# Kernel tuning notes

Hardware: AMD Instinct MI355X
Metric: run time of the kernel (lower is better)

## Reference

```python
import jax, jax.numpy as jnp
import numpy as np

D = 256          # input_dim
H = 4            # num_heads
W = 4            # window_size
NUM_SCALES = 3
FRACTAL = 2
NUM_CLASSES = 7


def _pool(t, ksize):
    # reflect-pad along time by ksize//2 each side, then avg_pool1d(kernel=stride=ksize)
    p = ksize // 2
    t = jnp.pad(t, ((0, 0), (p, p), (0, 0)), mode='reflect')
    B, Tp, F = t.shape
    L = Tp // ksize
    return t[:, :L * ksize].reshape(B, L, ksize, F).mean(axis=2)


def _window_attn(q, k, v):
    # windowed multi-head self-attention with zero-pad to a multiple of W
    B, T, F = q.shape
    pad = (-T) % W
    if pad:
        q = jnp.pad(q, ((0, 0), (0, pad), (0, 0)))
        k = jnp.pad(k, ((0, 0), (0, pad), (0, 0)))
        v = jnp.pad(v, ((0, 0), (0, pad), (0, 0)))
    Tp = T + pad
    nw = Tp // W
    hd = F // H
    scale = 1.0 / np.sqrt(hd).astype(np.float32)
    # [B, nw, W, H, hd] -> [B, nw, H, W, hd]
    qh = q.reshape(B, nw, W, H, hd).transpose(0, 1, 3, 2, 4)
    kh = k.reshape(B, nw, W, H, hd).transpose(0, 1, 3, 2, 4)
    vh = v.reshape(B, nw, W, H, hd).transpose(0, 1, 3, 2, 4)
    attn = jnp.einsum('bnhqd,bnhkd->bnhqk', qh, kh) * scale
    attn = jax.nn.softmax(attn, axis=-1)
    out = jnp.einsum('bnhqk,bnhkd->bnhqd', attn, vh)
    out = out.transpose(0, 1, 3, 2, 4).reshape(B, Tp, F)
    return out[:, :T]


def _upsample_nearest(f, out_len):
    # matches torch F.interpolate(mode='nearest'): src = floor(i * in / out)
    in_len = f.shape[1]
    idx = jnp.minimum((jnp.arange(out_len) * in_len) // out_len, in_len - 1)
    return f[:, idx]


def setup_inputs() -> dict:
    key = jax.random.key(0)
    ks = jax.random.split(key, 14)
    s = 1.0 / np.sqrt(D).astype(np.float32)
    inp = {
        'x': jax.random.normal(ks[0], (32, 4096, D), dtype=jnp.float32),
        'Wq': jax.random.normal(ks[1], (D, D), dtype=jnp.float32) * s,
        'bq': jnp.zeros((D,), jnp.float32),
        'Wk': jax.random.normal(ks[2], (D, D), dtype=jnp.float32) * s,
        'bk': jnp.zeros((D,), jnp.float32),
        'Wv': jax.random.normal(ks[3], (D, D), dtype=jnp.float32) * s,
        'bv': jnp.zeros((D,), jnp.float32),
        'Wp': jax.random.normal(ks[4], (D, D), dtype=jnp.float32) * s,
        'bp': jnp.zeros((D,), jnp.float32),
        'Wc1': jax.random.normal(ks[5], (D, D), dtype=jnp.float32) * s,
        'bc1': jnp.zeros((D,), jnp.float32),
        'Wc2': jax.random.normal(ks[6], (D, NUM_CLASSES), dtype=jnp.float32) * s,
        'bc2': jnp.zeros((NUM_CLASSES,), jnp.float32),
    }
    return inp


def reference(x, Wq, bq, Wk, bk, Wv, bv, Wp, bp, Wc1, bc1, Wc2, bc2):
    B, T, F = x.shape
    q = x @ Wq + bq
    k = x @ Wk + bk
    v = x @ Wv + bv
    # multi-scale temporal operator + per-scale fractal windowed attention
    outs = []
    for s_idx in range(1, NUM_SCALES + 1):
        ksize = FRACTAL ** (s_idx - 1)
        if ksize == 1:
            qs, ks_, vs = q, k, v
        else:
            qs, ks_, vs = _pool(q, ksize), _pool(k, ksize), _pool(v, ksize)
        outs.append(_window_attn(qs, ks_, vs))
    # scale mixer: nearest upsample + exact GELU + sum + proj
    summed = sum(jax.nn.gelu(_upsample_nearest(f, T), approximate=False) for f in outs)
    fused = summed @ Wp + bp
    # classifier (dropout inactive in eval)
    h = fused.mean(axis=1)
    h = jax.nn.relu(h @ Wc1 + bc1)
    logits = h @ Wc2 + bc2
    return logits
```

## Files before the change

### kernel.cpp

```cpp
#include <hip/hip_runtime.h>

#define DD 256
#define TT 4096
#define BB 32

typedef __attribute__((ext_vector_type(8))) short short8;
typedef __attribute__((ext_vector_type(4))) float floatx4;

__device__ __forceinline__ unsigned short f2bf(float f) {
    unsigned u = __builtin_bit_cast(unsigned, f);
    unsigned r = u + 0x7FFFu + ((u >> 16) & 1u);
    return (unsigned short)(r >> 16);
}
__device__ __forceinline__ float bf2f(unsigned short h) {
    return __builtin_bit_cast(float, (unsigned)h << 16);
}
__device__ __forceinline__ float2 unpk(unsigned u) {
    float2 r;
    r.x = __builtin_bit_cast(float, u << 16);
    r.y = __builtin_bit_cast(float, u & 0xFFFF0000u);
    return r;
}

#define GLDS16(g, l)                                                        \
    __builtin_amdgcn_global_load_lds(                                       \
        (const __attribute__((address_space(1))) void*)(g),                 \
        (__attribute__((address_space(3))) void*)(l), 16, 0, 0)

__global__ __launch_bounds__(256)
void prep_kernel(const float* __restrict__ X,
                 const float* __restrict__ Wq, const float* __restrict__ Wk,
                 const float* __restrict__ Wv,
                 unsigned short* __restrict__ Xp, unsigned short* __restrict__ Wt,
                 float* __restrict__ acc)
{
    const int bid = blockIdx.x;
    const int tid = threadIdx.x;
    if (bid < 16384) {
        size_t i = ((size_t)bid * 256 + tid) * 8;
        float4 a = *(const float4*)(X + i);
        float4 b = *(const float4*)(X + i + 4);
        short8 o;
        o[0] = (short)f2bf(a.x); o[1] = (short)f2bf(a.y);
        o[2] = (short)f2bf(a.z); o[3] = (short)f2bf(a.w);
        o[4] = (short)f2bf(b.x); o[5] = (short)f2bf(b.y);
        o[6] = (short)f2bf(b.z); o[7] = (short)f2bf(b.w);
        size_t row = i >> 8;
        int k = (int)(i & 255);
        size_t off = (size_t)(k >> 5) * (131072u * 32u) + row * 32 + (k & 31);
        *(short8*)(Xp + off) = o;
    } else if (bid < 16384 + 768) {
        const int wb = bid - 16384;
        const int z = wb >> 8;
        const int k = wb & 255;
        const int n = tid;
        const float* W = (z == 0) ? Wq : (z == 1) ? Wk : Wv;
        float w = W[k * 256 + n];
        unsigned short hi = f2bf(w);
        unsigned short lo = f2bf(w - bf2f(hi));
        size_t base = (size_t)z * 131072;
        size_t off = (size_t)(k >> 5) * 8192 + (size_t)n * 32 + (k & 31);
        Wt[base +         off] = hi;
        Wt[base + 65536 + off] = lo;
    } else {
        for (int i = tid; i < BB * DD; i += 256) acc[i] = 0.f;
    }
}

__global__ __launch_bounds__(256, 3)
void qkv_mfma_kernel(const unsigned short* __restrict__ Xp,
                     const unsigned short* __restrict__ Wt,
                     const float* __restrict__ bq, const float* __restrict__ bk,
                     const float* __restrict__ bv,
                     unsigned short* __restrict__ Q, unsigned short* __restrict__ Kp,
                     unsigned short* __restrict__ V)
{
    const int d = blockIdx.x;
    const int x = d & 7, t = d >> 3;
    const int m = t / 6, zc = t - 6 * m;
    const int z = zc >> 1;
    const int col0 = (zc & 1) * 128;
    const size_t row0 = (size_t)(x + 8 * m) * 128;

    const unsigned short* Wz = Wt + (size_t)z * 131072;
    const float* bias = (z == 0) ? bq : (z == 1) ? bk : bv;
    unsigned short* Y = (z == 0) ? Q : (z == 1) ? Kp : V;

    __shared__ __align__(16) unsigned char smem[49152];

    const int tid = threadIdx.x;
    const int lane = tid & 63, wave = tid >> 6;
    const int wm = wave & 1, wn = wave >> 1;
    const int l15 = lane & 15, lq = lane >> 4;

    floatx4 acc[4][4];
    #pragma unroll
    for (int i = 0; i < 4; ++i)
        #pragma unroll
        for (int j = 0; j < 4; ++j)
            acc[i][j] = (floatx4){0.f, 0.f, 0.f, 0.f};

    auto stage = [&](int p, int pb) {
        unsigned short* As = (unsigned short*)(smem + pb * 8192);
        unsigned short* Bs = (unsigned short*)(smem + 16384 + pb * 16384);
        const unsigned short* Ap = Xp + (size_t)p * (131072u * 32u);
        const unsigned short* Bp = Wz + (size_t)p * 8192;
        #pragma unroll
        for (int it = 0; it < 2; ++it) {
            int flat = it * 256 + tid;
            int mm = flat >> 2, c = flat & 3;
            int sc = c ^ ((mm >> 1) & 3);
            GLDS16(Ap + (row0 + mm) * 32 + sc * 8, As + flat * 8);
        }
        #pragma unroll
        for (int half = 0; half < 2; ++half)
            #pragma unroll
            for (int it = 0; it < 2; ++it) {
                int flat = it * 256 + tid;
                int n = flat >> 2, c = flat & 3;
                int sc = c ^ ((n >> 1) & 3);
                GLDS16(Bp + half * 65536 + (size_t)(col0 + n) * 32 + sc * 8,
                       Bs + half * 4096 + flat * 8);
            }
    };

    stage(0, 0);
    __syncthreads();

    for (int k = 0; k < 8; ++k) {
        const int pb = k & 1;
        if (k < 7) stage(k + 1, pb ^ 1);

        const unsigned short* As = (const unsigned short*)(smem + pb * 8192);
        const unsigned short* Bs = (const unsigned short*)(smem + 16384 + pb * 16384);

        short8 a[4];
        #pragma unroll
        for (int mt = 0; mt < 4; ++mt) {
            int row = wm * 64 + mt * 16 + l15;
            a[mt] = *(const short8*)(As + row * 32 + (lq ^ ((row >> 1) & 3)) * 8);
        }
        #pragma unroll
        for (int nt = 0; nt < 4; ++nt) {
            int nr = wn * 64 + nt * 16 + l15;
            const unsigned short* bp = Bs + nr * 32 + (lq ^ ((nr >> 1) & 3)) * 8;
            short8 bh = *(const short8*)bp;
            short8 bl = *(const short8*)(bp + 4096);
            #pragma unroll
            for (int mt = 0; mt < 4; ++mt) {
                acc[mt][nt] = __builtin_amdgcn_mfma_f32_16x16x32_bf16(a[mt], bh, acc[mt][nt], 0, 0, 0);
                acc[mt][nt] = __builtin_amdgcn_mfma_f32_16x16x32_bf16(a[mt], bl, acc[mt][nt], 0, 0, 0);
            }
        }
        __syncthreads();
    }

    unsigned short* Cs = (unsigned short*)(smem + wave * 8192);
    #pragma unroll
    for (int nt = 0; nt < 4; ++nt) {
        float bv_ = bias[col0 + wn * 64 + nt * 16 + l15];
        #pragma unroll
        for (int mt = 0; mt < 4; ++mt)
            #pragma unroll
            for (int r = 0; r < 4; ++r) {
                int row = mt * 16 + lq * 4 + r;
                Cs[row * 64 + nt * 16 + l15] = f2bf(acc[mt][nt][r] + bv_);
            }
    }
    #pragma unroll
    for (int p = 0; p < 8; ++p) {
        int row = p * 8 + (lane >> 3);
        float4 dd = *(const float4*)(Cs + row * 64 + (lane & 7) * 8);
        *(float4*)(Y + (row0 + wm * 64 + row) * 256 + col0 + wn * 64 + (lane & 7) * 8) = dd;
    }
}

__device__ __forceinline__ float gelu2(float x) {
    float z = fabsf(x) * 0.70710678118654752f;
    float t = __builtin_amdgcn_rcpf(fmaf(z, 0.3275911f, 1.0f));
    float p = fmaf(t, 1.061405429f, -1.453152027f);
    p = fmaf(p, t, 1.421413741f);
    p = fmaf(p, t, -0.284496736f);
    p = fmaf(p, t, 0.254829592f);
    p = p * t;
    float e = __expf(-z * z);
    float erf_abs = fmaf(-p, e, 1.0f);
    float erfv = copysignf(erf_abs, x);
    return x * (1.0f + erfv);
}
__device__ __forceinline__ void addu4(uint4 d, float* f) {
    float2 t;
    t = unpk(d.x); f[0] += t.x; f[1] += t.y;
    t = unpk(d.y); f[2] += t.x; f[3] += t.y;
    t = unpk(d.z); f[4] += t.x; f[5] += t.y;
    t = unpk(d.w); f[6] += t.x; f[7] += t.y;
}

#define SPAN 32
#define NROW 34

template<int KS>
__device__ __forceinline__ void pool_qk(const unsigned short* __restrict__ qb,
                                        const unsigned short* __restrict__ kb,
                                        int rp,
                                        float* __restrict__ qf,
                                        float* __restrict__ kf)
{
    #pragma unroll
    for (int j = 0; j < KS; ++j) {
        int ra = (rp >> (8 * j)) & 0xFF;
        uint4 qd = *(const uint4*)(qb + ra * 256);
        uint4 kd = *(const uint4*)(kb + ra * 256);
        addu4(qd, qf);
        addu4(kd, kf);
    }
}

template<int KS>
__device__ __forceinline__ void pool_v(const unsigned short* __restrict__ vb,
                                       int rp, float* __restrict__ vf)
{
    #pragma unroll
    for (int j = 0; j < KS; ++j) {
        int ra = (rp >> (8 * j)) & 0xFF;
        uint4 vd = *(const uint4*)(vb + ra * 256);
        addu4(vd, vf);
    }
}

template<int KS>
__device__ __forceinline__ void fast_unit(const unsigned short* __restrict__ qkvs,
                                          int rowbase,
                                          const float* __restrict__ cwh,
                                          float sscale, float inv_k, int fperm,
                                          float* __restrict__ accL)
{
    float S[4][4];
    #pragma unroll
    for (int i = 0; i < 4; ++i)
        #pragma unroll
        for (int j = 0; j < 4; ++j) S[i][j] = 0.f;

    #pragma unroll
    for (int half = 0; half < 2; ++half) {
        const unsigned short* qb = qkvs + half * 128 + fperm + rowbase * 256;
        const unsigned short* kb = qb + NROW * 256;
        float qf[4][8], kf[4][8];
        #pragma unroll
        for (int i = 0; i < 4; ++i) {
            #pragma unroll
            for (int e = 0; e < 8; ++e) { qf[i][e] = 0.f; kf[i][e] = 0.f; }
            #pragma unroll
            for (int j = 0; j < KS; ++j) {
                addu4(*(const uint4*)(qb + (i * KS + j) * 256), qf[i]);
                addu4(*(const uint4*)(kb + (i * KS + j) * 256), kf[i]);
            }
        }
        #pragma unroll
        for (int i = 0; i < 4; ++i)
            #pragma unroll
            for (int j = 0; j < 4; ++j) {
                float d = 0.f;
                #pragma unroll
                for (int e = 0; e < 8; ++e) d = fmaf(qf[i][e], kf[j][e], d);
                S[i][j] += d;
            }
    }
    #pragma unroll
    for (int i = 0; i < 4; ++i)
        #pragma unroll
        for (int j = 0; j < 4; ++j) {
            float t = S[i][j];
            t += __shfl_xor(t, 1, 64);
            t += __shfl_xor(t, 2, 64);
            S[i][j] = t * sscale;
        }
    float P[4][4];
    #pragma unroll
    for (int i = 0; i < 4; ++i) {
        float m = fmaxf(fmaxf(S[i][0], S[i][1]), fmaxf(S[i][2], S[i][3]));
        float e0 = __expf(S[i][0] - m), e1 = __expf(S[i][1] - m);
        float e2 = __expf(S[i][2] - m), e3 = __expf(S[i][3] - m);
        float inv = inv_k * __builtin_amdgcn_rcpf(e0 + e1 + e2 + e3);
        P[i][0] = e0 * inv; P[i][1] = e1 * inv; P[i][2] = e2 * inv; P[i][3] = e3 * inv;
    }
    #pragma unroll
    for (int half = 0; half < 2; ++half) {
        const unsigned short* vb =
            qkvs + 2 * NROW * 256 + half * 128 + fperm + rowbase * 256;
        float vf[4][8];
        #pragma unroll
        for (int i = 0; i < 4; ++i) {
            #pragma unroll
            for (int e = 0; e < 8; ++e) vf[i][e] = 0.f;
            #pragma unroll
            for (int j = 0; j < KS; ++j)
                addu4(*(const uint4*)(vb + (i * KS + j) * 256), vf[i]);
        }
        #pragma unroll
        for (int i = 0; i < 4; ++i) {
            #pragma unroll
            for (int e = 0; e < 8; ++e) {
                float o = P[i][0]*vf[0][e] + P[i][1]*vf[1][e]
                        + P[i][2]*vf[2][e] + P[i][3]*vf[3][e];
                accL[half * 8 + e] += cwh[i] * gelu2(o);
            }
        }
    }
}

__global__ __launch_bounds__(256, 3)
void attn_fused_kernel(const unsigned short* __restrict__ Q,
                       const unsigned short* __restrict__ K,
                       const unsigned short* __restrict__ V,
                       float* __restrict__ acc)
{
    __shared__ __align__(16) unsigned char smem[3 * NROW * 256 * 2];
    unsigned short* qkvs = (unsigned short*)smem;
    float* scratch = (float*)smem;

    const int tid = threadIdx.x;
    const int s = blockIdx.x;
    const int b = blockIdx.y;
    const int r0 = s * SPAN;
    const int rbase = r0 - 2;

    #pragma unroll
    for (int t = 0; t < 3; ++t) {
        const unsigned short* src =
            ((t == 0) ? Q : (t == 1) ? K : V) + (size_t)b * TT * DD;
        #pragma unroll
        for (int it = 0; it < 5; ++it) {
            int flat = it * 256 + tid;
            if (flat < NROW * 32) {
                int row = flat >> 5, dc = flat & 31;
                int g = rbase + row;
                g = (g < 0) ? 0 : g;
                int c = (((dc >> 2) & 3) << 3) | ((dc & 3) << 1) | ((dc >> 4) & 1);
                GLDS16(src + (size_t)g * DD + c * 8,
                       qkvs + t * (NROW * 256) + flat * 8);
            }
        }
    }
    __syncthreads();

    const int slot = tid >> 2, lq = tid & 3;
    const int head = slot & 3, u = slot >> 2;
    int ksize, LEN, w; bool active = true;
    if (u < 8)       { ksize = 1; LEN = 4096; w = s * 8 + u; }
    else if (u < 12) { ksize = 2; LEN = 2049; w = s * 4 + (u - 8); }
    else if (u < 14) { ksize = 4; LEN = 1025; w = s * 2 + (u - 12); }
    else if (u == 14){ ksize = 2; LEN = 2049; w = 512; active = (s == 127); }
    else             { ksize = 4; LEN = 1025; w = 256; active = (s == 127); }

    const int f0 = head * 64 + lq * 16;
    const int fperm = head * 32 + lq * 8;

    float accL[16];
    #pragma unroll
    for (int e = 0; e < 16; ++e) accL[e] = 0.f;

    const bool generic = (s == 0) || (s == 127);

    if (!generic) {
        if (active) {
            float cwh[4];
            if (ksize == 1) {
                #pragma unroll
                for (int i = 0; i < 4; ++i) cwh[i] = 0.5f;
                fast_unit<1>(qkvs, u * 4 + 2, cwh, 0.125f, 1.0f, fperm, accL);
            } else if (ksize == 2) {
                #pragma unroll
                for (int i = 0; i < 4; ++i) {
                    int p = 16 * s + 4 * (u - 8) + i;
                    cwh[i] = 0.5f * (float)(((p + 1) * TT + 2048) / 2049
                                          - (p * TT + 2048) / 2049);
                }
                fast_unit<2>(qkvs, 8 * (u - 8) + 1, cwh, 0.03125f, 0.5f, fperm, accL);
            } else {
                #pragma unroll
                for (int i = 0; i < 4; ++i) {
                    int p = 8 * s + 4 * (u - 12) + i;
                    cwh[i] = 0.5f * (float)(((p + 1) * TT + 1024) / 1025
                                          - (p * TT + 1024) / 1025);
                }
                fast_unit<4>(qkvs, 16 * (u - 12), cwh, 0.0078125f, 0.25f, fperm, accL);
            }
        }
    } else if (active) {
        int rp[4]; float cwh[4]; int vmask = 0;
        for (int i = 0; i < 4; ++i) {
            int p = w * 4 + i;
            bool vv = (p < LEN);
            if (vv) vmask |= (1 << i);
            int pc = vv ? p : 0;
            int r[4] = {0, 0, 0, 0};
            if (ksize == 1) { r[0] = pc; }
            else if (ksize == 2) {
                if (pc == 0)            { r[0] = 0;      r[1] = 1;      }
                else if (pc == LEN - 1) { r[0] = TT - 2; r[1] = TT - 1; }
                else                    { r[0] = 2 * pc - 1; r[1] = 2 * pc; }
            } else {
                if (pc == 0)            { r[0] = 2; r[1] = 1; r[2] = 0; r[3] = 1; }
                else if (pc == LEN - 1) { r[0] = TT - 3; r[1] = TT - 2; r[2] = TT - 2; r[3] = TT - 1; }
                else                    { r[0] = 4*pc - 2; r[1] = 4*pc - 1; r[2] = 4*pc; r[3] = 4*pc + 1; }
            }
            int rr = 0;
            #pragma unroll
            for (int j = 0; j < 4; ++j) rr |= ((r[j] - rbase) & 0xFF) << (8 * j);
            rp[i] = rr;
            float c = 0.5f;
            if (ksize == 2)
                c = 0.5f * (float)(((p + 1) * TT + 2048) / 2049 - (p * TT + 2048) / 2049);
            else if (ksize == 4)
                c = 0.5f * (float)(((p + 1) * TT + 1024) / 1025 - (p * TT + 1024) / 1025);
            cwh[i] = vv ? c : 0.f;
        }
        const float inv_k = 1.0f / (float)ksize;
        const float sscale = 0.125f * inv_k * inv_k;

        float S[4][4];
        #pragma unroll
        for (int i = 0; i < 4; ++i)
            #pragma unroll
            for (int j = 0; j < 4; ++j) S[i][j] = 0.f;

        for (int half = 0; half < 2; ++half) {
            float qf[4][8], kf[4][8];
            const unsigned short* qb = qkvs + half * 128 + fperm;
            const unsigned short* kb = qb + NROW * 256;
            #pragma unroll
            for (int i = 0; i < 4; ++i) {
                #pragma unroll
                for (int e = 0; e < 8; ++e) { qf[i][e] = 0.f; kf[i][e] = 0.f; }
                if (vmask & (1 << i)) {
                    if (ksize == 1)      pool_qk<1>(qb, kb, rp[i], qf[i], kf[i]);
                    else if (ksize == 2) pool_qk<2>(qb, kb, rp[i], qf[i], kf[i]);
                    else                 pool_qk<4>(qb, kb, rp[i], qf[i], kf[i]);
                }
            }
            #pragma unroll
            for (int i = 0; i < 4; ++i)
                #pragma unroll
                for (int j = 0; j < 4; ++j) {
                    float d = 0.f;
                    #pragma unroll
                    for (int e = 0; e < 8; ++e) d = fmaf(qf[i][e], kf[j][e], d);
                    S[i][j] += d;
                }
        }
        #pragma unroll
        for (int i = 0; i < 4; ++i)
            #pragma unroll
            for (int j = 0; j < 4; ++j) {
                float t = S[i][j];
                t += __shfl_xor(t, 1, 64);
                t += __shfl_xor(t, 2, 64);
                S[i][j] = t * sscale;
            }
        float P[4][4];
        #pragma unroll
        for (int i = 0; i < 4; ++i) {
            float m = fmaxf(fmaxf(S[i][0], S[i][1]), fmaxf(S[i][2], S[i][3]));
            float e0 = __expf(S[i][0] - m), e1 = __expf(S[i][1] - m);
            float e2 = __expf(S[i][2] - m), e3 = __expf(S[i][3] - m);
            float inv = inv_k * __builtin_amdgcn_rcpf(e0 + e1 + e2 + e3);
            P[i][0] = e0 * inv; P[i][1] = e1 * inv; P[i][2] = e2 * inv; P[i][3] = e3 * inv;
        }
        for (int half = 0; half < 2; ++half) {
            float vf[4][8];
            const unsigned short* vb = qkvs + 2 * NROW * 256 + half * 128 + fperm;
            #pragma unroll
            for (int i = 0; i < 4; ++i) {
                #pragma unroll
                for (int e = 0; e < 8; ++e) vf[i][e] = 0.f;
                if (vmask & (1 << i)) {
                    if (ksize == 1)      pool_v<1>(vb, rp[i], vf[i]);
                    else if (ksize == 2) pool_v<2>(vb, rp[i], vf[i]);
                    else                 pool_v<4>(vb, rp[i], vf[i]);
                }
            }
            #pragma unroll
            for (int i = 0; i < 4; ++i) {
                if (!(vmask & (1 << i))) continue;
                #pragma unroll
                for (int e = 0; e < 8; ++e) {
                    float o = P[i][0]*vf[0][e] + P[i][1]*vf[1][e]
                            + P[i][2]*vf[2][e] + P[i][3]*vf[3][e];
                    accL[half * 8 + e] += cwh[i] * gelu2(o);
                }
            }
        }
    }

    __syncthreads();
    #pragma unroll
    for (int e = 0; e < 16; e += 4) {
        float4 d = {accL[e], accL[e+1], accL[e+2], accL[e+3]};
        *(float4*)(scratch + u * 256 + f0 + e) = d;
    }
    __syncthreads();
    float sum = 0.f;
    #pragma unroll
    for (int uu = 0; uu < 16; ++uu) sum += scratch[uu * 256 + tid];
    atomicAdd(&acc[b * DD + tid], sum);
}

__global__ __launch_bounds__(256)
void classifier_kernel(const float* __restrict__ acc,
                       const float* __restrict__ Wp,  const float* __restrict__ bp,
                       const float* __restrict__ Wc1, const float* __restrict__ bc1,
                       const float* __restrict__ Wc2, const float* __restrict__ bc2,
                       float* __restrict__ out)
{
    const int b = blockIdx.x;
    const int d = threadIdx.x;
    __shared__ float sm[256], sf[256], sh[256];

    sm[d] = acc[b * 256 + d] * (1.0f / 4096.0f);
    __syncthreads();

    float s = bp[d];
    for (int kk = 0; kk < 256; ++kk) s = fmaf(sm[kk], Wp[kk * 256 + d], s);
    sf[d] = s;
    __syncthreads();

    s = bc1[d];
    for (int kk = 0; kk < 256; ++kk) s = fmaf(sf[kk], Wc1[kk * 256 + d], s);
    sh[d] = fmaxf(s, 0.0f);
    __syncthreads();

    if (d < 7) {
        s = bc2[d];
        for (int kk = 0; kk < 256; ++kk) s = fmaf(sh[kk], Wc2[kk * 7 + d], s);
        out[b * 7 + d] = s;
    }
}

extern "C" void kernel_launch(void* const* d_in, const int* in_sizes, int n_in,
                              void* d_out, int out_size, void* d_ws, size_t ws_size,
                              hipStream_t stream)
{
    const float* x   = (const float*)d_in[0];
    const float* Wq  = (const float*)d_in[1];
    const float* bq  = (const float*)d_in[2];
    const float* Wk  = (const float*)d_in[3];
    const float* bk  = (const float*)d_in[4];
    const float* Wv  = (const float*)d_in[5];
    const float* bv  = (const float*)d_in[6];
    const float* Wp  = (const float*)d_in[7];
    const float* bp  = (const float*)d_in[8];
    const float* Wc1 = (const float*)d_in[9];
    const float* bc1 = (const float*)d_in[10];
    const float* Wc2 = (const float*)d_in[11];
    const float* bc2 = (const float*)d_in[12];
    float* out = (float*)d_out;

    const size_t plane = (size_t)BB * TT * DD;
    unsigned short* Q  = (unsigned short*)d_ws;
    unsigned short* K  = Q + plane;
    unsigned short* V  = K + plane;
    unsigned short* Xh = V + plane;
    unsigned short* Wt = Xh + plane;
    float* acc = (float*)(Wt + 3 * 131072);

    prep_kernel<<<dim3(16384 + 768 + 1), 256, 0, stream>>>(
        x, Wq, Wk, Wv, Xh, Wt, acc);

    qkv_mfma_kernel<<<dim3(6144), 256, 0, stream>>>(
        Xh, Wt, bq, bk, bv, Q, K, V);

    attn_fused_kernel<<<dim3(128, BB), 256, 0, stream>>>(Q, K, V, acc);

    classifier_kernel<<<dim3(BB), 256, 0, stream>>>(acc, Wp, bp, Wc1, bc1, Wc2, bc2, out);
}
```

Baseline: 438.6 us.

## Split B hi/lo staging into half-steps to cut LDS and raise occupancy

Restructures the QKV MFMA GEMM pipeline so the hi and lo bf16 halves of the weight tile are staged into a single 8KB B buffer in alternating half-steps, instead of double-buffering both halves together. This drops shared memory from 48KB to 32KB and raises the launch-bounds occupancy hint from 3 to 4 blocks per CU, aiming to hide latency with more resident waves. In exchange, each k-step now has two barriers and less prefetch distance for B, so loads may be exposed. The change also reorders MFMA accumulation (all hi then all lo per k-step).

```diff
diff --git a/kernel.cpp b/kernel.cpp
--- a/kernel.cpp
+++ b/kernel.cpp
@@ -67,7 +67,7 @@
     }
 }
 
-__global__ __launch_bounds__(256, 3)
+__global__ __launch_bounds__(256, 4)
 void qkv_mfma_kernel(const unsigned short* __restrict__ Xp,
                      const unsigned short* __restrict__ Wt,
                      const float* __restrict__ bq, const float* __restrict__ bk,
@@ -86,7 +86,7 @@
     const float* bias = (z == 0) ? bq : (z == 1) ? bk : bv;
     unsigned short* Y = (z == 0) ? Q : (z == 1) ? Kp : V;
 
-    __shared__ __align__(16) unsigned char smem[49152];
+    __shared__ __align__(16) unsigned char smem[32768];
 
     const int tid = threadIdx.x;
     const int lane = tid & 63, wave = tid >> 6;
@@ -100,40 +100,32 @@
         for (int j = 0; j < 4; ++j)
             acc[i][j] = (floatx4){0.f, 0.f, 0.f, 0.f};
 
-    auto stage = [&](int p, int pb) {
-        unsigned short* As = (unsigned short*)(smem + pb * 8192);
-        unsigned short* Bs = (unsigned short*)(smem + 16384 + pb * 16384);
-        const unsigned short* Ap = Xp + (size_t)p * (131072u * 32u);
-        const unsigned short* Bp = Wz + (size_t)p * 8192;
+    auto stageA = [&](int p, int ap) {
+        unsigned short* As = (unsigned short*)(smem + ap * 8192);
+        const unsigned short* Apt = Xp + (size_t)p * (131072u * 32u);
         #pragma unroll
         for (int it = 0; it < 2; ++it) {
             int flat = it * 256 + tid;
             int mm = flat >> 2, c = flat & 3;
             int sc = c ^ ((mm >> 1) & 3);
-            GLDS16(Ap + (row0 + mm) * 32 + sc * 8, As + flat * 8);
-        }
-        #pragma unroll
-        for (int half = 0; half < 2; ++half)
-            #pragma unroll
-            for (int it = 0; it < 2; ++it) {
-                int flat = it * 256 + tid;
-                int n = flat >> 2, c = flat & 3;
-                int sc = c ^ ((n >> 1) & 3);
-                GLDS16(Bp + half * 65536 + (size_t)(col0 + n) * 32 + sc * 8,
-                       Bs + half * 4096 + flat * 8);
-            }
+            GLDS16(Apt + (row0 + mm) * 32 + sc * 8, As + flat * 8);
+        }
     };
-
-    stage(0, 0);
-    __syncthreads();
-
-    for (int k = 0; k < 8; ++k) {
-        const int pb = k & 1;
-        if (k < 7) stage(k + 1, pb ^ 1);
-
-        const unsigned short* As = (const unsigned short*)(smem + pb * 8192);
-        const unsigned short* Bs = (const unsigned short*)(smem + 16384 + pb * 16384);
-
+    auto stageB = [&](int p, int half, int bp) {
+        unsigned short* Bs = (unsigned short*)(smem + 16384 + bp * 8192);
+        const unsigned short* Bp = Wz + (size_t)half * 65536 + (size_t)p * 8192;
+        #pragma unroll
+        for (int it = 0; it < 2; ++it) {
+            int flat = it * 256 + tid;
+            int n = flat >> 2, c = flat & 3;
+            int sc = c ^ ((n >> 1) & 3);
+            GLDS16(Bp + (size_t)(col0 + n) * 32 + sc * 8, Bs + flat * 8);
+        }
+    };
+
+    auto compute = [&](int ap, int bp) {
+        const unsigned short* As = (const unsigned short*)(smem + ap * 8192);
+        const unsigned short* Bs = (const unsigned short*)(smem + 16384 + bp * 8192);
         short8 a[4];
         #pragma unroll
         for (int mt = 0; mt < 4; ++mt) {
@@ -143,15 +135,28 @@
         #pragma unroll
         for (int nt = 0; nt < 4; ++nt) {
             int nr = wn * 64 + nt * 16 + l15;
-            const unsigned short* bp = Bs + nr * 32 + (lq ^ ((nr >> 1) & 3)) * 8;
-            short8 bh = *(const short8*)bp;
-            short8 bl = *(const short8*)(bp + 4096);
-            #pragma unroll
-            for (int mt = 0; mt < 4; ++mt) {
-                acc[mt][nt] = __builtin_amdgcn_mfma_f32_16x16x32_bf16(a[mt], bh, acc[mt][nt], 0, 0, 0);
-                acc[mt][nt] = __builtin_amdgcn_mfma_f32_16x16x32_bf16(a[mt], bl, acc[mt][nt], 0, 0, 0);
-            }
-        }
+            short8 bfrag = *(const short8*)(Bs + nr * 32 + (lq ^ ((nr >> 1) & 3)) * 8);
+            #pragma unroll
+            for (int mt = 0; mt < 4; ++mt)
+                acc[mt][nt] = __builtin_amdgcn_mfma_f32_16x16x32_bf16(
+                    a[mt], bfrag, acc[mt][nt], 0, 0, 0);
+        }
+    };
+
+    stageA(0, 0);
+    stageB(0, 0, 0);
+    __syncthreads();
+
+    for (int p = 0; p < 8; ++p) {
+        const int ap = p & 1;
+        stageB(p, 1, 1);
+        compute(ap, 0);
+        __syncthreads();
+        if (p < 7) {
+            stageA(p + 1, ap ^ 1);
+            stageB(p + 1, 0, 0);
+        }
+        compute(ap, 1);
         __syncthreads();
     }
 
```

Measured after the change: 436.6 us. About the same (-0.5%).
